# Optimization experiments

Measured on AMD Instinct MI355X. Metric: run time of the kernel, lower is better.

## Reference

```python
import jax, jax.numpy as jnp
import numpy as np

EPS = 1e-5  # torch InstanceNorm2d default eps


def instance_norm(x):
    # normalize over spatial dims (H, W) per sample, per channel; affine=False
    mean = jnp.mean(x, axis=(2, 3), keepdims=True)
    var = jnp.var(x, axis=(2, 3), keepdims=True)  # biased var, matching torch
    return (x - mean) * jax.lax.rsqrt(var + EPS)


def conv1x1(x, w, b):
    # x: [B,C,H,W], w: [O,C], b: [O] -> [B,O,H,W]
    return jnp.einsum('oc,bchw->bohw', w, x) + b[None, :, None, None]


def setup_inputs() -> dict:
    key = jax.random.key(0)
    ks = jax.random.split(key, 9)
    B, C, H, W = 4, 64, 96, 96
    fan_out = C  # 1x1 conv: fan_out = out_ch * 1 * 1
    std = float(np.sqrt(2.0 / fan_out))  # kaiming_normal_, mode='fan_out', relu
    x = jax.random.normal(ks[0], (B, C, H, W), dtype=jnp.float32)
    wq = jax.random.normal(ks[1], (C, C), dtype=jnp.float32) * std
    wk = jax.random.normal(ks[2], (C, C), dtype=jnp.float32) * std
    wv = jax.random.normal(ks[3], (C, C), dtype=jnp.float32) * std
    wo = jax.random.normal(ks[4], (C, C), dtype=jnp.float32) * std
    bq = jnp.zeros((C,), dtype=jnp.float32)
    bk = jnp.zeros((C,), dtype=jnp.float32)
    bv = jnp.zeros((C,), dtype=jnp.float32)
    bo = jnp.zeros((C,), dtype=jnp.float32)
    return {"x": x, "wq": wq, "bq": bq, "wk": wk, "bk": bk,
            "wv": wv, "bv": bv, "wo": wo, "bo": bo}


def reference(x, wq, bq, wk, bk, wv, bv, wo, bo):
    B, C, H, W = x.shape
    h = instance_norm(x)
    q = conv1x1(h, wq, bq)  # [B,C,H,W]
    k = conv1x1(h, wk, bk)
    v = conv1x1(h, wv, bv)
    N = H * W
    q = q.reshape(B, C, N).transpose(0, 2, 1)  # [B,N,C]
    k = k.reshape(B, C, N)                     # [B,C,N]
    v = v.reshape(B, C, N).transpose(0, 2, 1)  # [B,N,C]
    scores = jnp.einsum('bnc,bcm->bnm', q, k) * (C ** -0.5)  # [B,N,N]
    attn = jax.nn.softmax(scores, axis=-1)
    o = jnp.einsum('bnm,bmc->bnc', attn, v)  # [B,N,C]
    o = o.reshape(B, H, W, C).transpose(0, 3, 1, 2)  # [B,C,H,W]
    o = conv1x1(o, wo, bo)
    return x + o
```

## Files before the change

kernel.cpp:

```cpp
#include <hip/hip_runtime.h>
#include <stdint.h>

#define BB 4
#define CCH 64
#define NN 9216
#define NTILES 144
#define FTILES 36
#define NCHUNK 5

typedef unsigned short u16;
typedef __attribute__((ext_vector_type(8))) short bhalf8;
typedef __attribute__((ext_vector_type(4))) float f32x4;
typedef __attribute__((ext_vector_type(4))) u16 u16x4;
typedef __attribute__((ext_vector_type(8))) u16 u16x8;
typedef __attribute__((ext_vector_type(2))) unsigned int u32x2;

#define MFMA16(a, b, c) __builtin_amdgcn_mfma_f32_16x16x32_bf16((a), (b), (c), 0, 0, 0)

static __device__ __forceinline__ u16 f2bf(float f) {
  union { float f; unsigned u; } v; v.f = f;
  return (u16)((v.u + 0x7fffu + ((v.u >> 16) & 1u)) >> 16);
}
static __device__ __forceinline__ float bf2f(u16 h) {
  union { unsigned u; float f; } v; v.u = ((unsigned)h) << 16; return v.f;
}
static __device__ __forceinline__ unsigned pk2(float lo, float hi) {
  unsigned a = __float_as_uint(hi) + 0x8000u;
  unsigned b = __float_as_uint(lo) + 0x8000u;
  return __builtin_amdgcn_perm(a, b, 0x07060302u);
}
static __device__ __forceinline__ void glds16(const void* g, void* l) {
  __builtin_amdgcn_global_load_lds(
      (const __attribute__((address_space(1))) unsigned int*)g,
      (__attribute__((address_space(3))) unsigned int*)l, 16, 0, 0);
}

extern "C" __global__ __launch_bounds__(256) void prep_kernel(
    const float* __restrict__ x,
    const float* __restrict__ wq, const float* __restrict__ wk,
    const float* __restrict__ wv, const float* __restrict__ wo,
    float* __restrict__ mean, float* __restrict__ rstd, u16* __restrict__ wbf) {
  if (blockIdx.x >= 256) {
    int i = (blockIdx.x - 256) * 256 + threadIdx.x;
    const float* src = (i < 4096) ? wq : (i < 8192) ? wk : (i < 12288) ? wv : wo;
    wbf[i] = f2bf(src[i & 4095]);
    return;
  }
  int idx = blockIdx.x;
  const float* p = x + (size_t)idx * NN;
  float s = 0.f, ss = 0.f;
  for (int i = threadIdx.x; i < NN; i += 256) { float v = p[i]; s += v; ss += v * v; }
#pragma unroll
  for (int o = 32; o > 0; o >>= 1) { s += __shfl_xor(s, o, 64); ss += __shfl_xor(ss, o, 64); }
  __shared__ float ls[4], lss[4];
  int w = threadIdx.x >> 6;
  if ((threadIdx.x & 63) == 0) { ls[w] = s; lss[w] = ss; }
  __syncthreads();
  if (threadIdx.x == 0) {
    s = ls[0] + ls[1] + ls[2] + ls[3];
    ss = lss[0] + lss[1] + lss[2] + lss[3];
    float m = s * (1.f / NN);
    float var = ss * (1.f / NN) - m * m;
    mean[idx] = m;
    rstd[idx] = rsqrtf(var + 1e-5f);
  }
}

extern "C" __global__ __launch_bounds__(256, 4) void qkv_kernel(
    const float* __restrict__ x,
    const float* __restrict__ mean, const float* __restrict__ rstd,
    const u16* __restrict__ wqb, const u16* __restrict__ wkb, const u16* __restrict__ wvb,
    const float* __restrict__ bq, const float* __restrict__ bk,
    u16* __restrict__ Qt, u16* __restrict__ Kt, u16* __restrict__ Vt) {
  __shared__ u16 hbuf[64 * 72];
  int b = blockIdx.x / NTILES, tile = blockIdx.x % NTILES;
  int n0 = tile * 64;
  int t = threadIdx.x;
  int w = t >> 6, lane = t & 63, q = lane >> 4, ln = lane & 15;
  const float QSCALE = 0.125f * 1.44269504088896340736f;
  const float* mb = mean + b * 64;
  const float* rb_ = rstd + b * 64;
  int nloc = lane;
#pragma unroll
  for (int rep = 0; rep < 4; rep++) {
    int c0 = 16 * w + 4 * rep;
    float h0 = (x[(size_t)(b * 64 + c0 + 0) * NN + n0 + nloc] - mb[c0 + 0]) * rb_[c0 + 0];
    float h1 = (x[(size_t)(b * 64 + c0 + 1) * NN + n0 + nloc] - mb[c0 + 1]) * rb_[c0 + 1];
    float h2 = (x[(size_t)(b * 64 + c0 + 2) * NN + n0 + nloc] - mb[c0 + 2]) * rb_[c0 + 2];
    float h3 = (x[(size_t)(b * 64 + c0 + 3) * NN + n0 + nloc] - mb[c0 + 3]) * rb_[c0 + 3];
    u32x2 hp;
    hp[0] = pk2(h0, h1);
    hp[1] = pk2(h2, h3);
    *(u32x2*)&hbuf[nloc * 72 + c0] = hp;
  }
  __syncthreads();
  int hrow = (16 * w + ln) * 72;
  bhalf8 hb0 = *(const bhalf8*)&hbuf[hrow + q * 8];
  bhalf8 hb1 = *(const bhalf8*)&hbuf[hrow + 32 + q * 8];
  size_t nrow = (size_t)(b * NN + n0 + 16 * w + ln) * 64;
#pragma unroll
  for (int ct = 0; ct < 4; ct++) {
    int wrow = (16 * ct + ln) * 64;
    bhalf8 a0 = *(const bhalf8*)&wqb[wrow + q * 8];
    bhalf8 a1 = *(const bhalf8*)&wqb[wrow + 32 + q * 8];
    f32x4 d = {0.f, 0.f, 0.f, 0.f};
    d = MFMA16(a0, hb0, d);
    d = MFMA16(a1, hb1, d);
    f32x4 b4 = *(const f32x4*)&bq[16 * ct + 4 * q];
    u16x4 pk;
#pragma unroll
    for (int r = 0; r < 4; r++) pk[r] = f2bf((d[r] + b4[r]) * QSCALE);
    *(u16x4*)&Qt[nrow + 16 * ct + 4 * q] = pk;
  }
#pragma unroll
  for (int ct = 0; ct < 4; ct++) {
    int wrow = (16 * ct + ln) * 64;
    bhalf8 a0 = *(const bhalf8*)&wkb[wrow + q * 8];
    bhalf8 a1 = *(const bhalf8*)&wkb[wrow + 32 + q * 8];
    f32x4 d = {0.f, 0.f, 0.f, 0.f};
    d = MFMA16(a0, hb0, d);
    d = MFMA16(a1, hb1, d);
    f32x4 b4 = *(const f32x4*)&bk[16 * ct + 4 * q];
    u16x4 pk;
#pragma unroll
    for (int r = 0; r < 4; r++) pk[r] = f2bf(d[r] + b4[r]);
    *(u16x4*)&Kt[nrow + 16 * ct + 4 * q] = pk;
  }
#pragma unroll
  for (int ct = 0; ct < 4; ct++) {
    int wrow = (16 * ct + ln) * 64;
    bhalf8 b0 = *(const bhalf8*)&wvb[wrow + q * 8];
    bhalf8 b1 = *(const bhalf8*)&wvb[wrow + 32 + q * 8];
    f32x4 d = {0.f, 0.f, 0.f, 0.f};
    d = MFMA16(hb0, b0, d);
    d = MFMA16(hb1, b1, d);
    u16x4 pk;
#pragma unroll
    for (int r = 0; r < 4; r++) pk[r] = f2bf(d[r]);
    *(u16x4*)&Vt[(size_t)(b * 64 + 16 * ct + ln) * NN + n0 + 16 * w + 4 * q] = pk;
  }
}

extern "C" __global__ __launch_bounds__(256, 3) void flash_kernel(
    const u16* __restrict__ Qt, const u16* __restrict__ Kt, const u16* __restrict__ Vt,
    u16* __restrict__ Opart, float* __restrict__ Lsum) {
  __shared__ u16 kbuf[2][64 * 64];
  __shared__ u16 vbuf[2][64 * 64];
  __shared__ u16 pbuf[4][64 * 32];
  int blk = blockIdx.x;
  int b = blk / (FTILES * NCHUNK);
  int rem = blk % (FTILES * NCHUNK);
  int tile = rem / NCHUNK, chunk = rem % NCHUNK;
  int it0 = chunk * 28 + (chunk < 4 ? chunk : 4);
  int nit = 28 + (chunk < 4 ? 1 : 0);
  int m_start = it0 * 64;
  int t = threadIdx.x;
  int w = t >> 6, lane = t & 63, q = lane >> 4, ln = lane & 15;
  int n0w = tile * 256 + 64 * w;
  bhalf8 qf0[4], qf1[4];
#pragma unroll
  for (int s = 0; s < 4; s++) {
    const u16* qp = Qt + (size_t)(b * NN + n0w + 16 * s + ln) * 64 + q * 8;
    qf0[s] = *(const bhalf8*)qp;
    qf1[s] = *(const bhalf8*)(qp + 32);
  }
  const short ONE = 0x3F80;
  const bhalf8 ones = {ONE, ONE, ONE, ONE, ONE, ONE, ONE, ONE};
  f32x4 o[4][4];
  f32x4 lacc[4];
#pragma unroll
  for (int ct = 0; ct < 4; ct++) {
    lacc[ct] = (f32x4){0.f, 0.f, 0.f, 0.f};
#pragma unroll
    for (int s = 0; s < 4; s++) o[ct][s] = (f32x4){0.f, 0.f, 0.f, 0.f};
  }
  u16* pw = pbuf[w];
  int row_s = 16 * w + (lane >> 3);
  int usw = (lane & 7) ^ (row_s & 7);
  const u16* kgp = Kt + ((size_t)b * NN + m_start + row_s) * 64 + usw * 8;
  const u16* vgp = Vt + (size_t)(b * 64 + row_s) * NN + m_start + usw * 8;
  int sbase = (q ^ (ln & 7)) * 8;

  {
    u16* kl = &kbuf[0][w * 1024];
    u16* vl = &vbuf[0][w * 1024];
    glds16(kgp, kl); glds16(kgp + 512, kl + 512);
    glds16(vgp, vl); glds16(vgp + (size_t)8 * NN, vl + 512);
    kgp += 4096; vgp += 64;
  }

  for (int i = 0; i < nit; i++) {
    __syncthreads();
    if (i + 1 < nit) {
      u16* kl = &kbuf[(i + 1) & 1][w * 1024];
      u16* vl = &vbuf[(i + 1) & 1][w * 1024];
      glds16(kgp, kl); glds16(kgp + 512, kl + 512);
      glds16(vgp, vl); glds16(vgp + (size_t)8 * NN, vl + 512);
      kgp += 4096; vgp += 64;
    }
    const u16* kb = kbuf[i & 1];
    const u16* vb = vbuf[i & 1];
#pragma unroll
    for (int p = 0; p < 2; p++) {
#pragma unroll
      for (int lm = 0; lm < 2; lm++) {
        int krow = (16 * (2 * p + lm) + ln) * 64;
        bhalf8 ka0 = *(const bhalf8*)&kb[krow + sbase];
        bhalf8 ka1 = *(const bhalf8*)&kb[krow + (sbase ^ 32)];
        int uw = (((2 * lm + (q >> 1)) ^ ((ln >> 1) & 3)) << 3) + ((q & 1) << 2);
#pragma unroll
        for (int s = 0; s < 4; s++) {
          f32x4 acc = {0.f, 0.f, 0.f, 0.f};
          acc = MFMA16(ka0, qf0[s], acc);
          acc = MFMA16(ka1, qf1[s], acc);
          f32x4 pv;
#pragma unroll
          for (int r = 0; r < 4; r++) pv[r] = __builtin_amdgcn_exp2f(acc[r]);
          u32x2 pk;
          pk[0] = pk2(pv[0], pv[1]);
          pk[1] = pk2(pv[2], pv[3]);
          *(u32x2*)&pw[(16 * s + ln) * 32 + uw] = pk;
        }
      }
      int ur = ((q ^ ((ln >> 1) & 3)) << 3);
      bhalf8 pf[4];
#pragma unroll
      for (int s = 0; s < 4; s++) pf[s] = *(const bhalf8*)&pw[(16 * s + ln) * 32 + ur];
#pragma unroll
      for (int s = 0; s < 4; s++) lacc[s] = MFMA16(ones, pf[s], lacc[s]);
#pragma unroll
      for (int ct = 0; ct < 4; ct++) {
        bhalf8 va = *(const bhalf8*)&vb[(16 * ct + ln) * 64 + (sbase ^ (32 * p))];
#pragma unroll
        for (int s = 0; s < 4; s++) o[ct][s] = MFMA16(va, pf[s], o[ct][s]);
      }
    }
  }
  size_t pbase = (size_t)blk * (256 * 64);
#pragma unroll
  for (int s = 0; s < 4; s++) {
    int row = 64 * w + 16 * s + ln;
#pragma unroll
    for (int ct = 0; ct < 4; ct++) {
      u32x2 pk;
      pk[0] = pk2(o[ct][s][0], o[ct][s][1]);
      pk[1] = pk2(o[ct][s][2], o[ct][s][3]);
      *(u32x2*)&Opart[pbase + (size_t)row * 64 + 16 * ct + 4 * q] = pk;
    }
    if (q == 0) Lsum[(size_t)blk * 256 + row] = lacc[s][0];
  }
}

extern "C" __global__ __launch_bounds__(256, 4) void out_kernel(
    const float* __restrict__ x, const u16* __restrict__ wob, const float* __restrict__ bo,
    const u16* __restrict__ Opart, const float* __restrict__ Lsum, const float* __restrict__ bv,
    float* __restrict__ out) {
  int b = blockIdx.x / NTILES, tile = blockIdx.x % NTILES;
  int t = threadIdx.x;
  int w = t >> 6, lane = t & 63, q = lane >> 4, ln = lane & 15;
  int n0w = tile * 64 + 16 * w;
  int ptile = tile >> 2;
  int prow = (tile & 3) * 64 + 16 * w + ln;
  int p0 = (b * FTILES + ptile) * NCHUNK;
  float L = 0.f;
  float acc0[8], acc1[8];
#pragma unroll
  for (int j = 0; j < 8; j++) { acc0[j] = 0.f; acc1[j] = 0.f; }
#pragma unroll
  for (int ch = 0; ch < NCHUNK; ch++) {
    L += Lsum[(size_t)(p0 + ch) * 256 + prow];
    const u16* op = Opart + ((size_t)(p0 + ch) * 256 + prow) * 64;
    u16x8 d0 = *(const u16x8*)(op + 8 * q);
    u16x8 d1 = *(const u16x8*)(op + 32 + 8 * q);
#pragma unroll
    for (int j = 0; j < 8; j++) { acc0[j] += bf2f(d0[j]); acc1[j] += bf2f(d1[j]); }
  }
  float rl = 1.0f / L;
  union { u16x8 us; bhalf8 bh; } A0, A1;
#pragma unroll
  for (int j = 0; j < 8; j++) {
    A0.us[j] = f2bf(acc0[j] * rl + bv[8 * q + j]);
    A1.us[j] = f2bf(acc1[j] * rl + bv[32 + 8 * q + j]);
  }
  bhalf8 a0 = A0.bh, a1 = A1.bh;
#pragma unroll
  for (int ct = 0; ct < 4; ct++) {
    int wrow = (16 * ct + ln) * 64;
    bhalf8 b0 = *(const bhalf8*)&wob[wrow + q * 8];
    bhalf8 b1 = *(const bhalf8*)&wob[wrow + 32 + q * 8];
    f32x4 d = {0.f, 0.f, 0.f, 0.f};
    d = MFMA16(a0, b0, d);
    d = MFMA16(a1, b1, d);
    int co = 16 * ct + ln;
    size_t base = (size_t)(b * 64 + co) * NN + n0w + 4 * q;
    f32x4 xv = *(const f32x4*)&x[base];
    float bc = bo[co];
    f32x4 ov;
#pragma unroll
    for (int r = 0; r < 4; r++) ov[r] = xv[r] + bc + d[r];
    *(f32x4*)&out[base] = ov;
  }
}

extern "C" void kernel_launch(void* const* d_in, const int* in_sizes, int n_in,
                              void* d_out, int out_size, void* d_ws, size_t ws_size,
                              hipStream_t stream) {
  (void)in_sizes; (void)n_in; (void)out_size; (void)ws_size;
  const float* x  = (const float*)d_in[0];
  const float* wq = (const float*)d_in[1];
  const float* bq = (const float*)d_in[2];
  const float* wk = (const float*)d_in[3];
  const float* bk = (const float*)d_in[4];
  const float* wv = (const float*)d_in[5];
  const float* bv = (const float*)d_in[6];
  const float* wo = (const float*)d_in[7];
  const float* bo = (const float*)d_in[8];
  float* out = (float*)d_out;
  char* ws = (char*)d_ws;
  float* mean = (float*)ws;
  float* rstd = (float*)(ws + 1024);
  u16* wbf = (u16*)(ws + 2048);
  u16* Qt = (u16*)(ws + 36864);
  u16* Kt = Qt + (size_t)BB * NN * 64;
  u16* Vt = Kt + (size_t)BB * NN * 64;
  u16* Opart = Vt + (size_t)BB * NN * 64;
  float* Lsum = (float*)(Opart + (size_t)BB * FTILES * NCHUNK * 256 * 64);
  const u16* wqb = wbf;
  const u16* wkb = wbf + 4096;
  const u16* wvb = wbf + 8192;
  const u16* wob = wbf + 12288;

  prep_kernel<<<320, 256, 0, stream>>>(x, wq, wk, wv, wo, mean, rstd, wbf);
  qkv_kernel<<<BB * NTILES, 256, 0, stream>>>(x, mean, rstd, wqb, wkb, wvb, bq, bk, Qt, Kt, Vt);
  flash_kernel<<<BB * FTILES * NCHUNK, 256, 0, stream>>>(Qt, Kt, Vt, Opart, Lsum);
  out_kernel<<<BB * NTILES, 256, 0, stream>>>(x, wob, bo, Opart, Lsum, bv, out);
}
```

Measured before the change: 213.1 us.

## Halve flash query tile to 128 rows, drop K/V double buffering, vectorize stats

The flash kernel now runs 128-thread blocks, each covering 128 query rows instead of 256, which doubles the grid to 1440 blocks. K/V staging becomes single-buffered, with each wave loading 32 rows through four async copies and a barrier before compute. The aim is more blocks and less LDS per block for higher occupancy, at the cost of losing load/compute overlap inside a block and reading K/V twice as often overall. The prep kernel also switches to float4 loads for the instance-norm statistics.

Result: no change. 211.6 us (-0.7%).

```diff
diff --git a/kernel.cpp b/kernel.cpp
--- a/kernel.cpp
+++ b/kernel.cpp
@@ -5,7 +5,7 @@
 #define CCH 64
 #define NN 9216
 #define NTILES 144
-#define FTILES 36
+#define FTILES 72
 #define NCHUNK 5
 
 typedef unsigned short u16;
@@ -47,9 +47,13 @@
     return;
   }
   int idx = blockIdx.x;
-  const float* p = x + (size_t)idx * NN;
+  const f32x4* p4 = (const f32x4*)(x + (size_t)idx * NN);
   float s = 0.f, ss = 0.f;
-  for (int i = threadIdx.x; i < NN; i += 256) { float v = p[i]; s += v; ss += v * v; }
+  for (int i = threadIdx.x; i < NN / 4; i += 256) {
+    f32x4 v = p4[i];
+#pragma unroll
+    for (int j = 0; j < 4; j++) { s += v[j]; ss += v[j] * v[j]; }
+  }
 #pragma unroll
   for (int o = 32; o > 0; o >>= 1) { s += __shfl_xor(s, o, 64); ss += __shfl_xor(ss, o, 64); }
   __shared__ float ls[4], lss[4];
@@ -141,12 +145,12 @@
   }
 }
 
-extern "C" __global__ __launch_bounds__(256, 3) void flash_kernel(
+extern "C" __global__ __launch_bounds__(128, 3) void flash_kernel(
     const u16* __restrict__ Qt, const u16* __restrict__ Kt, const u16* __restrict__ Vt,
     u16* __restrict__ Opart, float* __restrict__ Lsum) {
-  __shared__ u16 kbuf[2][64 * 64];
-  __shared__ u16 vbuf[2][64 * 64];
-  __shared__ u16 pbuf[4][64 * 32];
+  __shared__ u16 kbuf[64 * 64];
+  __shared__ u16 vbuf[64 * 64];
+  __shared__ u16 pbuf[2][64 * 32];
   int blk = blockIdx.x;
   int b = blk / (FTILES * NCHUNK);
   int rem = blk % (FTILES * NCHUNK);
@@ -156,7 +160,7 @@
   int m_start = it0 * 64;
   int t = threadIdx.x;
   int w = t >> 6, lane = t & 63, q = lane >> 4, ln = lane & 15;
-  int n0w = tile * 256 + 64 * w;
+  int n0w = tile * 128 + 64 * w;
   bhalf8 qf0[4], qf1[4];
 #pragma unroll
   for (int s = 0; s < 4; s++) {
@@ -175,38 +179,31 @@
     for (int s = 0; s < 4; s++) o[ct][s] = (f32x4){0.f, 0.f, 0.f, 0.f};
   }
   u16* pw = pbuf[w];
-  int row_s = 16 * w + (lane >> 3);
-  int usw = (lane & 7) ^ (row_s & 7);
-  const u16* kgp = Kt + ((size_t)b * NN + m_start + row_s) * 64 + usw * 8;
-  const u16* vgp = Vt + (size_t)(b * 64 + row_s) * NN + m_start + usw * 8;
-  int sbase = (q ^ (ln & 7)) * 8;
-
-  {
-    u16* kl = &kbuf[0][w * 1024];
-    u16* vl = &vbuf[0][w * 1024];
-    glds16(kgp, kl); glds16(kgp + 512, kl + 512);
-    glds16(vgp, vl); glds16(vgp + (size_t)8 * NN, vl + 512);
-    kgp += 4096; vgp += 64;
-  }
+  int r0 = 32 * w + (lane >> 3);
+  int usw = (lane & 7) ^ (r0 & 7);
+  const u16* kgp = Kt + ((size_t)b * NN + m_start + r0) * 64 + usw * 8;
+  const u16* vgp = Vt + (size_t)(b * 64 + r0) * NN + m_start + usw * 8;
+  u16* klds = &kbuf[w * 2048];
+  u16* vlds = &vbuf[w * 2048];
+  int sbase = (q ^ (ln & 15 & 7)) * 8;
 
   for (int i = 0; i < nit; i++) {
     __syncthreads();
-    if (i + 1 < nit) {
-      u16* kl = &kbuf[(i + 1) & 1][w * 1024];
-      u16* vl = &vbuf[(i + 1) & 1][w * 1024];
-      glds16(kgp, kl); glds16(kgp + 512, kl + 512);
-      glds16(vgp, vl); glds16(vgp + (size_t)8 * NN, vl + 512);
-      kgp += 4096; vgp += 64;
+#pragma unroll
+    for (int k = 0; k < 4; k++) {
+      glds16(kgp + k * 512, klds + k * 512);
+      glds16(vgp + (size_t)(8 * k) * NN, vlds + k * 512);
     }
-    const u16* kb = kbuf[i & 1];
-    const u16* vb = vbuf[i & 1];
+    kgp += 4096;
+    vgp += 64;
+    __syncthreads();
 #pragma unroll
     for (int p = 0; p < 2; p++) {
 #pragma unroll
       for (int lm = 0; lm < 2; lm++) {
         int krow = (16 * (2 * p + lm) + ln) * 64;
-        bhalf8 ka0 = *(const bhalf8*)&kb[krow + sbase];
-        bhalf8 ka1 = *(const bhalf8*)&kb[krow + (sbase ^ 32)];
+        bhalf8 ka0 = *(const bhalf8*)&kbuf[krow + sbase];
+        bhalf8 ka1 = *(const bhalf8*)&kbuf[krow + (sbase ^ 32)];
         int uw = (((2 * lm + (q >> 1)) ^ ((ln >> 1) & 3)) << 3) + ((q & 1) << 2);
 #pragma unroll
         for (int s = 0; s < 4; s++) {
@@ -230,13 +227,13 @@
       for (int s = 0; s < 4; s++) lacc[s] = MFMA16(ones, pf[s], lacc[s]);
 #pragma unroll
       for (int ct = 0; ct < 4; ct++) {
-        bhalf8 va = *(const bhalf8*)&vb[(16 * ct + ln) * 64 + (sbase ^ (32 * p))];
+        bhalf8 va = *(const bhalf8*)&vbuf[(16 * ct + ln) * 64 + (sbase ^ (32 * p))];
 #pragma unroll
         for (int s = 0; s < 4; s++) o[ct][s] = MFMA16(va, pf[s], o[ct][s]);
       }
     }
   }
-  size_t pbase = (size_t)blk * (256 * 64);
+  size_t pbase = (size_t)blk * (128 * 64);
 #pragma unroll
   for (int s = 0; s < 4; s++) {
     int row = 64 * w + 16 * s + ln;
@@ -247,7 +244,7 @@
       pk[1] = pk2(o[ct][s][2], o[ct][s][3]);
       *(u32x2*)&Opart[pbase + (size_t)row * 64 + 16 * ct + 4 * q] = pk;
     }
-    if (q == 0) Lsum[(size_t)blk * 256 + row] = lacc[s][0];
+    if (q == 0) Lsum[(size_t)blk * 128 + row] = lacc[s][0];
   }
 }
 
@@ -259,8 +256,8 @@
   int t = threadIdx.x;
   int w = t >> 6, lane = t & 63, q = lane >> 4, ln = lane & 15;
   int n0w = tile * 64 + 16 * w;
-  int ptile = tile >> 2;
-  int prow = (tile & 3) * 64 + 16 * w + ln;
+  int ptile = tile >> 1;
+  int prow = (tile & 1) * 64 + 16 * w + ln;
   int p0 = (b * FTILES + ptile) * NCHUNK;
   float L = 0.f;
   float acc0[8], acc1[8];
@@ -268,8 +265,8 @@
   for (int j = 0; j < 8; j++) { acc0[j] = 0.f; acc1[j] = 0.f; }
 #pragma unroll
   for (int ch = 0; ch < NCHUNK; ch++) {
-    L += Lsum[(size_t)(p0 + ch) * 256 + prow];
-    const u16* op = Opart + ((size_t)(p0 + ch) * 256 + prow) * 64;
+    L += Lsum[(size_t)(p0 + ch) * 128 + prow];
+    const u16* op = Opart + ((size_t)(p0 + ch) * 128 + prow) * 64;
     u16x8 d0 = *(const u16x8*)(op + 8 * q);
     u16x8 d1 = *(const u16x8*)(op + 32 + 8 * q);
 #pragma unroll
@@ -324,7 +321,7 @@
   u16* Kt = Qt + (size_t)BB * NN * 64;
   u16* Vt = Kt + (size_t)BB * NN * 64;
   u16* Opart = Vt + (size_t)BB * NN * 64;
-  float* Lsum = (float*)(Opart + (size_t)BB * FTILES * NCHUNK * 256 * 64);
+  float* Lsum = (float*)(Opart + (size_t)BB * FTILES * NCHUNK * 128 * 64);
   const u16* wqb = wbf;
   const u16* wkb = wbf + 4096;
   const u16* wvb = wbf + 8192;
@@ -332,6 +329,6 @@
 
   prep_kernel<<<320, 256, 0, stream>>>(x, wq, wk, wv, wo, mean, rstd, wbf);
   qkv_kernel<<<BB * NTILES, 256, 0, stream>>>(x, mean, rstd, wqb, wkb, wvb, bq, bk, Qt, Kt, Vt);
-  flash_kernel<<<BB * FTILES * NCHUNK, 256, 0, stream>>>(Qt, Kt, Vt, Opart, Lsum);
+  flash_kernel<<<BB * FTILES * NCHUNK, 128, 0, stream>>>(Qt, Kt, Vt, Opart, Lsum);
   out_kernel<<<BB * NTILES, 256, 0, stream>>>(x, wob, bo, Opart, Lsum, bv, out);
 }
```
